# Kernel tuning notes

Hardware: AMD Instinct MI355X
Metric: run time of the kernel (lower is better)

Reference implementation:

```python
import jax, jax.numpy as jnp
import numpy as np

INPUT_SIZE = 512
HIDDEN_SIZE = 1024
OUTPUT_SIZE = 512
BATCH = 128
SEQ_LEN = 512


def setup_inputs() -> dict:
    key = jax.random.key(0)
    k_x, k_xh, k_hh, k_yh = jax.random.split(key, 4)

    def xavier(k, shape):
        fan_in, fan_out = shape
        lim = float(np.sqrt(6.0 / (fan_in + fan_out)))
        return jax.random.uniform(k, shape, jnp.float32, -lim, lim)

    return {
        "x": jax.random.normal(k_x, (BATCH, SEQ_LEN, INPUT_SIZE), jnp.float32),
        "W_xh": xavier(k_xh, (INPUT_SIZE, HIDDEN_SIZE)),
        "W_hh": xavier(k_hh, (HIDDEN_SIZE, HIDDEN_SIZE)),
        "W_yh": xavier(k_yh, (HIDDEN_SIZE, OUTPUT_SIZE)),
        "W_bh": jnp.zeros((HIDDEN_SIZE,), jnp.float32),
        "W_by": jnp.zeros((OUTPUT_SIZE,), jnp.float32),
    }


def reference(x, W_xh, W_hh, W_yh, W_bh, W_by):
    # x: [B, S, I]. Precompute input projections for all steps (parallel GEMM),
    # then scan the strictly sequential hidden recurrence.
    xW = jnp.einsum("bsi,ih->bsh", x, W_xh) + W_bh  # [B, S, H]
    h0 = jnp.zeros((x.shape[0], W_hh.shape[0]), x.dtype)

    def step(h, xw_t):
        h_new = jnp.tanh(xw_t + h @ W_hh)
        return h_new, None

    h_last, _ = jax.lax.scan(step, h0, jnp.swapaxes(xW, 0, 1))  # scan over S
    return h_last @ W_yh + W_by  # [B, O]
```

## Files before the change

kernel.cpp:

```cpp
#include <hip/hip_runtime.h>

typedef _Float16 half8 __attribute__((ext_vector_type(8)));
typedef float f32x4 __attribute__((ext_vector_type(4)));
typedef unsigned long long u64;
typedef u64 u64x2 __attribute__((ext_vector_type(2)));

#define MFMA16(a,b,c) __builtin_amdgcn_mfma_f32_16x16x32_f16((a),(b),(c),0,0,0)

constexpr int B_SZ = 128, S_LEN = 512, I_SZ = 512, H_SZ = 1024, O_SZ = 512;

constexpr size_t XW_OFF   = 0;
constexpr size_t X16_OFF  = XW_OFF   + (size_t)S_LEN * B_SZ * H_SZ * 2;
constexpr size_t WXHT_OFF = X16_OFF  + (size_t)B_SZ * S_LEN * I_SZ * 2;
constexpr size_t WHHT_OFF = WXHT_OFF + (size_t)H_SZ * I_SZ * 2;
constexpr size_t WYHT_OFF = WHHT_OFF + (size_t)H_SZ * H_SZ * 2;
constexpr size_t HB_OFF   = WYHT_OFF + (size_t)O_SZ * H_SZ * 2;
constexpr size_t TAG_OFF  = HB_OFF   + (size_t)8 * 8192 * 8;

__device__ __forceinline__ u64 ag_load64(const u64* p) {
  return __hip_atomic_load(p, __ATOMIC_RELAXED, __HIP_MEMORY_SCOPE_AGENT);
}
__device__ __forceinline__ void ag_store64(u64* p, u64 v) {
  __hip_atomic_store(p, v, __ATOMIC_RELAXED, __HIP_MEMORY_SCOPE_AGENT);
}
__device__ __forceinline__ unsigned ag_load32(const unsigned* p) {
  return __hip_atomic_load(p, __ATOMIC_RELAXED, __HIP_MEMORY_SCOPE_AGENT);
}
__device__ __forceinline__ void ag_store32(unsigned* p, unsigned v) {
  __hip_atomic_store(p, v, __ATOMIC_RELAXED, __HIP_MEMORY_SCOPE_AGENT);
}

__device__ __forceinline__ float ftanh(float z) {
  float e = __builtin_amdgcn_exp2f(z * 2.8853900817779268f);
  return fmaf(-2.f, __builtin_amdgcn_rcpf(e + 1.f), 1.f);
}

__global__ void k_cvt_x(const float* __restrict__ in, _Float16* __restrict__ out) {
  size_t i = ((size_t)blockIdx.x * 256 + threadIdx.x) * 8;
  float4 a = *(const float4*)(in + i);
  float4 b = *(const float4*)(in + i + 4);
  half8 h;
  h[0] = (_Float16)a.x; h[1] = (_Float16)a.y; h[2] = (_Float16)a.z; h[3] = (_Float16)a.w;
  h[4] = (_Float16)b.x; h[5] = (_Float16)b.y; h[6] = (_Float16)b.z; h[7] = (_Float16)b.w;
  *(half8*)(out + i) = h;
}

__global__ void k_transpose_cvt(const float* __restrict__ in, _Float16* __restrict__ out,
                                int K, int N) {
  int k = blockIdx.x * 256 + threadIdx.x;
  int n = blockIdx.y;
  out[(size_t)n * K + k] = (_Float16)in[(size_t)k * N + n];
}

__launch_bounds__(256, 1)
__global__ void k_xw_gemm(const _Float16* __restrict__ A,
                          const _Float16* __restrict__ BT,
                          const float* __restrict__ bias,
                          _Float16* __restrict__ xw)
{
  const int m0 = blockIdx.y * 128;
  const int n0 = blockIdx.x * 128;
  __shared__ __align__(16) _Float16 la[128][72];
  __shared__ __align__(16) _Float16 lb[128][72];
  const int tid = threadIdx.x;
  const int w = tid >> 6, l = tid & 63;
  const int wr = w >> 1, wc = w & 1;
  const int cl = l & 15;
  const int kh = (l >> 4) << 3;
  const int rl = (l >> 4) << 2;

  f32x4 acc[4][4] = {};

  for (int kb = 0; kb < 512; kb += 64) {
    {
      const int r = tid >> 1, sg = tid & 1;
      const _Float16* ga = A  + (size_t)(m0 + r) * 512 + kb + sg * 32;
      const _Float16* gb = BT + (size_t)(n0 + r) * 512 + kb + sg * 32;
      _Float16* da = &la[r][sg * 32];
      _Float16* db = &lb[r][sg * 32];
      #pragma unroll
      for (int i = 0; i < 4; i++) *(half8*)(da + i * 8) = *(const half8*)(ga + i * 8);
      #pragma unroll
      for (int i = 0; i < 4; i++) *(half8*)(db + i * 8) = *(const half8*)(gb + i * 8);
    }
    __syncthreads();
    #pragma unroll
    for (int kk = 0; kk < 64; kk += 32) {
      half8 af[4], bf[4];
      #pragma unroll
      for (int mi = 0; mi < 4; mi++) af[mi] = *(const half8*)(&la[wr * 64 + mi * 16 + cl][kk + kh]);
      #pragma unroll
      for (int ni = 0; ni < 4; ni++) bf[ni] = *(const half8*)(&lb[wc * 64 + ni * 16 + cl][kk + kh]);
      #pragma unroll
      for (int mi = 0; mi < 4; mi++)
        #pragma unroll
        for (int ni = 0; ni < 4; ni++)
          acc[mi][ni] = MFMA16(af[mi], bf[ni], acc[mi][ni]);
    }
    __syncthreads();
  }

  #pragma unroll
  for (int mi = 0; mi < 4; mi++)
    #pragma unroll
    for (int ni = 0; ni < 4; ni++) {
      const int col = n0 + wc * 64 + ni * 16 + cl;
      const float bv = bias[col];
      #pragma unroll
      for (int r = 0; r < 4; r++) {
        const int m = m0 + wr * 64 + mi * 16 + rl + r;
        const int b = m >> 9;
        const int s = m & 511;
        xw[((size_t)(s * B_SZ + b) << 10) + col] = (_Float16)(acc[mi][ni][r] + bv);
      }
    }
}


__device__ __forceinline__ void poll_tags(const unsigned* gtag, int l, unsigned t) {
  for (int it = 0; it < (1 << 17); ++it) {
    unsigned tg = ag_load32(gtag + (l & 31));
    if (__all((int)(tg >= t))) break;
    __builtin_amdgcn_s_sleep(1);
  }
  __builtin_amdgcn_sched_barrier(0);
}

template<int BLK0>
__device__ __forceinline__ void issueq8(u64 (&buf)[8][2], const u64* hrow) {
  #pragma unroll
  for (int b = 0; b < 8; b++) {
    buf[b][0] = ag_load64(hrow + ((BLK0 + b) << 7));
    buf[b][1] = ag_load64(hrow + ((BLK0 + b) << 7) + 1);
  }
}

template<int BLK0>
__device__ __forceinline__ void mfmaq8(const u64 (&buf)[8][2],
                                       const _Float16 (*lw)[1032],
                                       int w, int cl, int kh, f32x4 (&acc)[2][2]) {
  #pragma unroll
  for (int b = 0; b < 8; b++) {
    const int p = BLK0 + b;
    u64x2 w2 = { buf[b][0], buf[b][1] };
    half8 a = __builtin_bit_cast(half8, w2);
    half8 b0 = *(const half8*)&lw[(w << 5) + cl][(p << 5) + kh];
    half8 b1 = *(const half8*)&lw[(w << 5) + 16 + cl][(p << 5) + kh];
    acc[0][p & 1] = MFMA16(a, b0, acc[0][p & 1]);
    acc[1][p & 1] = MFMA16(a, b1, acc[1][p & 1]);
  }
}

template<int BLK0>
__device__ __forceinline__ void mfmaq_o8(const u64 (&buf)[8][2],
                                         const _Float16* bsrc,
                                         int kh, f32x4 (&oa)[2]) {
  #pragma unroll
  for (int b = 0; b < 8; b++) {
    const int p = BLK0 + b;
    u64x2 w2 = { buf[b][0], buf[b][1] };
    half8 a = __builtin_bit_cast(half8, w2);
    half8 bv = *(const half8*)(bsrc + (p << 5) + kh);
    oa[p & 1] = MFMA16(a, bv, oa[p & 1]);
  }
}

__launch_bounds__(128, 1)
__global__ void k_rnn(const _Float16* __restrict__ xw,
                      const _Float16* __restrict__ WhhT,
                      const _Float16* __restrict__ WyhT,
                      const float* __restrict__ Wby,
                      u64* __restrict__ hb,
                      unsigned* __restrict__ tags,
                      float* __restrict__ out)
{
  __shared__ __align__(16) _Float16 lw[64][1032];
  __shared__ __align__(16) _Float16 stb[2][16][40];

  const int bid = blockIdx.x;
  const int g = bid & 7, j = bid >> 3;
  const int tid = threadIdx.x;
  const int w = tid >> 6, l = tid & 63;
  const int p_self = (j << 1) | w;
  const int cl  = l & 15;
  const int kh  = (l >> 4) << 3;
  const int kh2 = (l >> 4) << 1;
  const int rl  = (l >> 4) << 2;
  const int r0  = g << 4;
  const int colbase = p_self << 5;
  unsigned* gtag = tags + (g << 5);
  u64* hbg = hb + ((size_t)g << 13);

  for (int i = tid; i < 64 * 128; i += 128) {
    const int row = i >> 7, c8 = (i & 127) << 3;
    *(half8*)&lw[row][c8] = *(const half8*)&WhhT[((size_t)((j << 6) + row) << 10) + c8];
  }
  __syncthreads();

  for (int t = 0; t < 512; t++) {
    float xv[2][4];
    {
      const _Float16* p = xw + ((size_t)(t * 128 + r0 + rl) << 10) + colbase + cl;
      #pragma unroll
      for (int f = 0; f < 2; f++)
        #pragma unroll
        for (int r = 0; r < 4; r++)
          xv[f][r] = (float)p[((size_t)r << 10) + (f << 4)];
    }

    f32x4 acc[2][2] = {{{}, {}}, {{}, {}}};
    if (t > 0) {
      poll_tags(gtag, l, (unsigned)t);
      const u64* hrow = hbg + ((size_t)(t & 1) << 12) + (cl << 3) + kh2;
      u64 qa[8][2], qb[8][2];
      issueq8<0>(qa, hrow);
      issueq8<8>(qb, hrow);
      mfmaq8<0>(qa, lw, w, cl, kh, acc);
      issueq8<16>(qa, hrow);
      mfmaq8<8>(qb, lw, w, cl, kh, acc);
      issueq8<24>(qb, hrow);
      mfmaq8<16>(qa, lw, w, cl, kh, acc);
      mfmaq8<24>(qb, lw, w, cl, kh, acc);
    }

    #pragma unroll
    for (int f = 0; f < 2; f++)
      #pragma unroll
      for (int r = 0; r < 4; r++) {
        float z = xv[f][r] + acc[f][0][r] + acc[f][1][r];
        stb[w][rl + r][(f << 4) + cl] = (_Float16)ftanh(z);
      }
    asm volatile("s_waitcnt lgkmcnt(0)" ::: "memory");
    __builtin_amdgcn_sched_barrier(0);
    {
      const u64* sp = (const u64*)&stb[w][l >> 2][(l & 3) << 3];
      u64 p0 = sp[0], p1 = sp[1];
      u64* dst = hbg + ((size_t)((t + 1) & 1) << 12) + (p_self << 7)
               + ((l >> 2) << 3) + ((l & 3) << 1);
      ag_store64(dst, p0);
      ag_store64(dst + 1, p1);
    }
    asm volatile("s_waitcnt vmcnt(0)" ::: "memory");
    if (l == 0) ag_store32(gtag + p_self, (unsigned)(t + 1));
  }

  poll_tags(gtag, l, 512u);
  {
    const u64* hrow = hbg + (cl << 3) + kh2;
    const int oc = (p_self << 4) + cl;
    const _Float16* bsrc = WyhT + ((size_t)oc << 10);
    f32x4 oa[2] = {{}, {}};
    u64 qa[8][2], qb[8][2];
    issueq8<0>(qa, hrow);
    issueq8<8>(qb, hrow);
    mfmaq_o8<0>(qa, bsrc, kh, oa);
    issueq8<16>(qa, hrow);
    mfmaq_o8<8>(qb, bsrc, kh, oa);
    issueq8<24>(qb, hrow);
    mfmaq_o8<16>(qa, bsrc, kh, oa);
    mfmaq_o8<24>(qb, bsrc, kh, oa);

    const float bb = Wby[oc];
    #pragma unroll
    for (int r = 0; r < 4; r++)
      out[((size_t)(r0 + rl + r) << 9) + oc] = oa[0][r] + oa[1][r] + bb;
  }
}

extern "C" void kernel_launch(void* const* d_in, const int* in_sizes, int n_in,
                              void* d_out, int out_size, void* d_ws, size_t ws_size,
                              hipStream_t stream) {
  const float* x   = (const float*)d_in[0];
  const float* Wxh = (const float*)d_in[1];
  const float* Whh = (const float*)d_in[2];
  const float* Wyh = (const float*)d_in[3];
  const float* Wbh = (const float*)d_in[4];
  const float* Wby = (const float*)d_in[5];
  float* out = (float*)d_out;

  char* ws = (char*)d_ws;
  _Float16* xw   = (_Float16*)(ws + XW_OFF);
  _Float16* x16  = (_Float16*)(ws + X16_OFF);
  _Float16* WxhT = (_Float16*)(ws + WXHT_OFF);
  _Float16* WhhT = (_Float16*)(ws + WHHT_OFF);
  _Float16* WyhT = (_Float16*)(ws + WYHT_OFF);
  u64*      hb   = (u64*)(ws + HB_OFF);
  unsigned* tags = (unsigned*)(ws + TAG_OFF);

  hipMemsetAsync(tags, 0, 8 * 32 * sizeof(unsigned), stream);

  k_cvt_x<<<16384, 256, 0, stream>>>(x, x16);
  k_transpose_cvt<<<dim3(2, 1024), 256, 0, stream>>>(Wxh, WxhT, 512, 1024);
  k_transpose_cvt<<<dim3(4, 1024), 256, 0, stream>>>(Whh, WhhT, 1024, 1024);
  k_transpose_cvt<<<dim3(4, 512),  256, 0, stream>>>(Wyh, WyhT, 1024, 512);

  k_xw_gemm<<<dim3(8, 512), 256, 0, stream>>>(x16, WxhT, Wbh, xw);

  k_rnn<<<128, 128, 0, stream>>>(xw, WhhT, WyhT, Wby, hb, tags, out);
}
```

Measured before the change: 1.977 ms.

## Consume hidden-state chunks as soon as their producer tags are ready

Replaces the all-or-nothing wait on 32 producer tags with a polling loop that checks readiness per group of 8 producers and issues the loads and MFMAs for each quarter of K as soon as its producers have published step t. Tags are also spread to 64-byte strides so each producer's flag sits on its own cache line, avoiding false sharing between writers. The aim is to overlap recurrent matmul work with waiting on slow blocks in the per-step cross-block barrier. The cost is dynamic control flow, with runtime-indexed helper functions and a polling loop that has no sleep. This may add register pressure and hurt instruction scheduling.

```diff
diff --git a/kernel.cpp b/kernel.cpp
--- a/kernel.cpp
+++ b/kernel.cpp
@@ -117,51 +117,39 @@
 }
 
 
-__device__ __forceinline__ void poll_tags(const unsigned* gtag, int l, unsigned t) {
-  for (int it = 0; it < (1 << 17); ++it) {
-    unsigned tg = ag_load32(gtag + (l & 31));
-    if (__all((int)(tg >= t))) break;
-    __builtin_amdgcn_s_sleep(1);
-  }
-  __builtin_amdgcn_sched_barrier(0);
-}
-
-template<int BLK0>
-__device__ __forceinline__ void issueq8(u64 (&buf)[8][2], const u64* hrow) {
+__device__ __forceinline__ void issueq8r(u64 (&buf)[8][2], const u64* hrow, int blk0) {
   #pragma unroll
   for (int b = 0; b < 8; b++) {
-    buf[b][0] = ag_load64(hrow + ((BLK0 + b) << 7));
-    buf[b][1] = ag_load64(hrow + ((BLK0 + b) << 7) + 1);
-  }
-}
-
-template<int BLK0>
-__device__ __forceinline__ void mfmaq8(const u64 (&buf)[8][2],
-                                       const _Float16 (*lw)[1032],
-                                       int w, int cl, int kh, f32x4 (&acc)[2][2]) {
+    buf[b][0] = ag_load64(hrow + ((blk0 + b) << 7));
+    buf[b][1] = ag_load64(hrow + ((blk0 + b) << 7) + 1);
+  }
+}
+
+__device__ __forceinline__ void mfmaq8r(const u64 (&buf)[8][2],
+                                        const _Float16 (*lw)[1032], int blk0,
+                                        int w, int cl, int kh, f32x4 (&acc)[2][2]) {
   #pragma unroll
   for (int b = 0; b < 8; b++) {
-    const int p = BLK0 + b;
+    const int p = blk0 + b;
     u64x2 w2 = { buf[b][0], buf[b][1] };
     half8 a = __builtin_bit_cast(half8, w2);
     half8 b0 = *(const half8*)&lw[(w << 5) + cl][(p << 5) + kh];
     half8 b1 = *(const half8*)&lw[(w << 5) + 16 + cl][(p << 5) + kh];
-    acc[0][p & 1] = MFMA16(a, b0, acc[0][p & 1]);
-    acc[1][p & 1] = MFMA16(a, b1, acc[1][p & 1]);
-  }
-}
-
-template<int BLK0>
-__device__ __forceinline__ void mfmaq_o8(const u64 (&buf)[8][2],
-                                         const _Float16* bsrc,
-                                         int kh, f32x4 (&oa)[2]) {
+    acc[0][b & 1] = MFMA16(a, b0, acc[0][b & 1]);
+    acc[1][b & 1] = MFMA16(a, b1, acc[1][b & 1]);
+  }
+}
+
+__device__ __forceinline__ void mfmaq_o8r(const u64 (&buf)[8][2],
+                                          const _Float16* bsrc, int blk0,
+                                          int kh, f32x4 (&oa)[2]) {
   #pragma unroll
   for (int b = 0; b < 8; b++) {
-    const int p = BLK0 + b;
+    const int p = blk0 + b;
     u64x2 w2 = { buf[b][0], buf[b][1] };
     half8 a = __builtin_bit_cast(half8, w2);
     half8 bv = *(const half8*)(bsrc + (p << 5) + kh);
-    oa[p & 1] = MFMA16(a, bv, oa[p & 1]);
+    oa[b & 1] = MFMA16(a, bv, oa[b & 1]);
   }
 }
 
@@ -188,7 +176,8 @@
   const int rl  = (l >> 4) << 2;
   const int r0  = g << 4;
   const int colbase = p_self << 5;
-  unsigned* gtag = tags + (g << 5);
+  unsigned* gtag = tags + (g << 9);
+  const unsigned* tp = gtag + ((l & 31) << 4);
   u64* hbg = hb + ((size_t)g << 13);
 
   for (int i = tid; i < 64 * 128; i += 128) {
@@ -210,17 +199,23 @@
 
     f32x4 acc[2][2] = {{{}, {}}, {{}, {}}};
     if (t > 0) {
-      poll_tags(gtag, l, (unsigned)t);
       const u64* hrow = hbg + ((size_t)(t & 1) << 12) + (cl << 3) + kh2;
       u64 qa[8][2], qb[8][2];
-      issueq8<0>(qa, hrow);
-      issueq8<8>(qb, hrow);
-      mfmaq8<0>(qa, lw, w, cl, kh, acc);
-      issueq8<16>(qa, hrow);
-      mfmaq8<8>(qb, lw, w, cl, kh, acc);
-      issueq8<24>(qb, hrow);
-      mfmaq8<16>(qa, lw, w, cl, kh, acc);
-      mfmaq8<24>(qb, lw, w, cl, kh, acc);
+      unsigned done = 0;
+      for (int it = 0; done != 0xFu && it < (1 << 17); ++it) {
+        unsigned tg = ag_load32(tp);
+        unsigned rdy = (unsigned)__ballot((int)(tg >= (unsigned)t));
+        unsigned n01 = 0, n23 = 0;
+        if (!(done & 1u) && ((rdy & 0x000000FFu) == 0x000000FFu)) { issueq8r(qa, hrow, 0);  n01 |= 1u; }
+        if (!(done & 2u) && ((rdy & 0x0000FF00u) == 0x0000FF00u)) { issueq8r(qb, hrow, 8);  n01 |= 2u; }
+        if (n01 & 1u) mfmaq8r(qa, lw, 0,  w, cl, kh, acc);
+        if (n01 & 2u) mfmaq8r(qb, lw, 8,  w, cl, kh, acc);
+        if (!(done & 4u) && ((rdy & 0x00FF0000u) == 0x00FF0000u)) { issueq8r(qa, hrow, 16); n23 |= 1u; }
+        if (!(done & 8u) && ((rdy & 0xFF000000u) == 0xFF000000u)) { issueq8r(qb, hrow, 24); n23 |= 2u; }
+        if (n23 & 1u) mfmaq8r(qa, lw, 16, w, cl, kh, acc);
+        if (n23 & 2u) mfmaq8r(qb, lw, 24, w, cl, kh, acc);
+        done |= (n01 & 3u) | ((n23 & 3u) << 2);
+      }
     }
 
     #pragma unroll
@@ -241,24 +236,29 @@
       ag_store64(dst + 1, p1);
     }
     asm volatile("s_waitcnt vmcnt(0)" ::: "memory");
-    if (l == 0) ag_store32(gtag + p_self, (unsigned)(t + 1));
-  }
-
-  poll_tags(gtag, l, 512u);
+    if (l == 0) ag_store32(gtag + (p_self << 4), (unsigned)(t + 1));
+  }
+
+  for (int it = 0; it < (1 << 17); ++it) {
+    unsigned tg = ag_load32(tp);
+    if (((unsigned)__ballot((int)(tg >= 512u))) == 0xFFFFFFFFu) break;
+    __builtin_amdgcn_s_sleep(1);
+  }
+  __builtin_amdgcn_sched_barrier(0);
   {
     const u64* hrow = hbg + (cl << 3) + kh2;
     const int oc = (p_self << 4) + cl;
     const _Float16* bsrc = WyhT + ((size_t)oc << 10);
     f32x4 oa[2] = {{}, {}};
     u64 qa[8][2], qb[8][2];
-    issueq8<0>(qa, hrow);
-    issueq8<8>(qb, hrow);
-    mfmaq_o8<0>(qa, bsrc, kh, oa);
-    issueq8<16>(qa, hrow);
-    mfmaq_o8<8>(qb, bsrc, kh, oa);
-    issueq8<24>(qb, hrow);
-    mfmaq_o8<16>(qa, bsrc, kh, oa);
-    mfmaq_o8<24>(qb, bsrc, kh, oa);
+    issueq8r(qa, hrow, 0);
+    issueq8r(qb, hrow, 8);
+    mfmaq_o8r(qa, bsrc, 0, kh, oa);
+    issueq8r(qa, hrow, 16);
+    mfmaq_o8r(qb, bsrc, 8, kh, oa);
+    issueq8r(qb, hrow, 24);
+    mfmaq_o8r(qa, bsrc, 16, kh, oa);
+    mfmaq_o8r(qb, bsrc, 24, kh, oa);
 
     const float bb = Wby[oc];
     #pragma unroll
@@ -287,7 +287,7 @@
   u64*      hb   = (u64*)(ws + HB_OFF);
   unsigned* tags = (unsigned*)(ws + TAG_OFF);
 
-  hipMemsetAsync(tags, 0, 8 * 32 * sizeof(unsigned), stream);
+  hipMemsetAsync(tags, 0, 8 * 32 * 16 * sizeof(unsigned), stream);
 
   k_cvt_x<<<16384, 256, 0, stream>>>(x, x16);
   k_transpose_cvt<<<dim3(2, 1024), 256, 0, stream>>>(Wxh, WxhT, 512, 1024);
```

After: 2.109 ms. 6.6% more time.

## Detect same-XCD groups and use L2-coherent sc0 loads for recurrence sync

Applied to the files above, without the earlier changes.

Each block records its XCC ID. If all 16 blocks of a batch group share one XCD, the group switches to a fast path. That path polls tags and loads the hidden state with sc0 global loads, which are coherent within the shared L2. It also batches 16-byte loads before issuing the MFMAs. This aims to cut per-step cross-block synchronization latency compared with agent-scope atomics, and falls back to the old path on a timeout or a mixed-XCD placement. It relies on block-to-XCD placement and on cache-coherence details, so a wrong assumption would make reads stale.

```diff
diff --git a/kernel.cpp b/kernel.cpp
--- a/kernel.cpp
+++ b/kernel.cpp
@@ -16,6 +16,7 @@
 constexpr size_t WYHT_OFF = WHHT_OFF + (size_t)H_SZ * H_SZ * 2;
 constexpr size_t HB_OFF   = WYHT_OFF + (size_t)O_SZ * H_SZ * 2;
 constexpr size_t TAG_OFF  = HB_OFF   + (size_t)8 * 8192 * 8;
+constexpr size_t XCDS_OFF = TAG_OFF  + 1024;
 
 __device__ __forceinline__ u64 ag_load64(const u64* p) {
   return __hip_atomic_load(p, __ATOMIC_RELAXED, __HIP_MEMORY_SCOPE_AGENT);
@@ -28,6 +29,18 @@
 }
 __device__ __forceinline__ void ag_store32(unsigned* p, unsigned v) {
   __hip_atomic_store(p, v, __ATOMIC_RELAXED, __HIP_MEMORY_SCOPE_AGENT);
+}
+
+__device__ __forceinline__ unsigned ld_tag_sc0(const unsigned* p) {
+  unsigned v;
+  asm volatile("global_load_dword %0, %1, off sc0\n\ts_waitcnt vmcnt(0)"
+               : "=v"(v) : "v"(p) : "memory");
+  return v;
+}
+__device__ __forceinline__ u64x2 ld_x4_sc0(const u64* p) {
+  u64x2 v;
+  asm volatile("global_load_dwordx4 %0, %1, off sc0" : "=v"(v) : "v"(p) : "memory");
+  return v;
 }
 
 __device__ __forceinline__ float ftanh(float z) {
@@ -117,7 +130,7 @@
 }
 
 
-__device__ __forceinline__ void poll_tags(const unsigned* gtag, int l, unsigned t) {
+__device__ __forceinline__ void poll_tags_ag(const unsigned* gtag, int l, unsigned t) {
   for (int it = 0; it < (1 << 17); ++it) {
     unsigned tg = ag_load32(gtag + (l & 31));
     if (__all((int)(tg >= t))) break;
@@ -165,6 +178,27 @@
   }
 }
 
+template<int BLK0>
+__device__ __forceinline__ void fast_half(const u64* hrow,
+                                          const _Float16 (*lw)[1032],
+                                          int w, int cl, int kh, f32x4 (&acc)[2][2]) {
+  u64x2 hq[16];
+  #pragma unroll
+  for (int p = 0; p < 16; p++) hq[p] = ld_x4_sc0(hrow + ((BLK0 + p) << 7));
+  asm volatile("s_waitcnt vmcnt(0)" ::: "memory");
+  __builtin_amdgcn_sched_barrier(0);
+  #pragma unroll
+  for (int p = 0; p < 16; p++) {
+    const int pb = BLK0 + p;
+    half8 a  = __builtin_bit_cast(half8, hq[p]);
+    half8 b0 = *(const half8*)&lw[(w << 5) + cl][(pb << 5) + kh];
+    half8 b1 = *(const half8*)&lw[(w << 5) + 16 + cl][(pb << 5) + kh];
+    acc[0][p & 1] = MFMA16(a, b0, acc[0][p & 1]);
+    acc[1][p & 1] = MFMA16(a, b1, acc[1][p & 1]);
+  }
+  __builtin_amdgcn_sched_barrier(0);
+}
+
 __launch_bounds__(128, 1)
 __global__ void k_rnn(const _Float16* __restrict__ xw,
                       const _Float16* __restrict__ WhhT,
@@ -172,6 +206,7 @@
                       const float* __restrict__ Wby,
                       u64* __restrict__ hb,
                       unsigned* __restrict__ tags,
+                      unsigned* __restrict__ xcds,
                       float* __restrict__ out)
 {
   __shared__ __align__(16) _Float16 lw[64][1032];
@@ -189,13 +224,33 @@
   const int r0  = g << 4;
   const int colbase = p_self << 5;
   unsigned* gtag = tags + (g << 5);
+  const unsigned* tp = gtag + (l & 31);
   u64* hbg = hb + ((size_t)g << 13);
+
+  if (tid == 0) {
+    unsigned xcc;
+    asm volatile("s_getreg_b32 %0, hwreg(HW_REG_XCC_ID)" : "=s"(xcc));
+    ag_store32(xcds + (g << 4) + j, (xcc & 7u) + 1u);
+  }
 
   for (int i = tid; i < 64 * 128; i += 128) {
     const int row = i >> 7, c8 = (i & 127) << 3;
     *(half8*)&lw[row][c8] = *(const half8*)&WhhT[((size_t)((j << 6) + row) << 10) + c8];
   }
   __syncthreads();
+
+  bool fast;
+  {
+    unsigned v = 0;
+    bool all_set = false;
+    for (int it = 0; it < (1 << 18) && !all_set; ++it) {
+      v = (l < 16) ? ag_load32(xcds + (g << 4) + l) : 1u;
+      all_set = __all((int)(v != 0u));
+      if (!all_set) __builtin_amdgcn_s_sleep(4);
+    }
+    unsigned v0 = __shfl(v, 0);
+    fast = all_set && __all((int)(l < 16 ? (v == v0) : 1));
+  }
 
   for (int t = 0; t < 512; t++) {
     float xv[2][4];
@@ -210,17 +265,35 @@
 
     f32x4 acc[2][2] = {{{}, {}}, {{}, {}}};
     if (t > 0) {
-      poll_tags(gtag, l, (unsigned)t);
       const u64* hrow = hbg + ((size_t)(t & 1) << 12) + (cl << 3) + kh2;
-      u64 qa[8][2], qb[8][2];
-      issueq8<0>(qa, hrow);
-      issueq8<8>(qb, hrow);
-      mfmaq8<0>(qa, lw, w, cl, kh, acc);
-      issueq8<16>(qa, hrow);
-      mfmaq8<8>(qb, lw, w, cl, kh, acc);
-      issueq8<24>(qb, hrow);
-      mfmaq8<16>(qa, lw, w, cl, kh, acc);
-      mfmaq8<24>(qb, lw, w, cl, kh, acc);
+      bool consumed = false;
+      if (fast) {
+        bool ok = false;
+        for (int it = 0; it < (1 << 14); ++it) {
+          unsigned tg = ld_tag_sc0(tp);
+          if (__all((int)(tg >= (unsigned)t))) { ok = true; break; }
+        }
+        if (ok) {
+          __builtin_amdgcn_sched_barrier(0);
+          fast_half<0>(hrow, lw, w, cl, kh, acc);
+          fast_half<16>(hrow, lw, w, cl, kh, acc);
+          consumed = true;
+        } else {
+          fast = false;
+        }
+      }
+      if (!consumed) {
+        poll_tags_ag(gtag, l, (unsigned)t);
+        u64 qa[8][2], qb[8][2];
+        issueq8<0>(qa, hrow);
+        issueq8<8>(qb, hrow);
+        mfmaq8<0>(qa, lw, w, cl, kh, acc);
+        issueq8<16>(qa, hrow);
+        mfmaq8<8>(qb, lw, w, cl, kh, acc);
+        issueq8<24>(qb, hrow);
+        mfmaq8<16>(qa, lw, w, cl, kh, acc);
+        mfmaq8<24>(qb, lw, w, cl, kh, acc);
+      }
     }
 
     #pragma unroll
@@ -244,7 +317,7 @@
     if (l == 0) ag_store32(gtag + p_self, (unsigned)(t + 1));
   }
 
-  poll_tags(gtag, l, 512u);
+  poll_tags_ag(gtag, l, 512u);
   {
     const u64* hrow = hbg + (cl << 3) + kh2;
     const int oc = (p_self << 4) + cl;
@@ -287,7 +360,7 @@
   u64*      hb   = (u64*)(ws + HB_OFF);
   unsigned* tags = (unsigned*)(ws + TAG_OFF);
 
-  hipMemsetAsync(tags, 0, 8 * 32 * sizeof(unsigned), stream);
+  hipMemsetAsync(tags, 0, 1536, stream);
 
   k_cvt_x<<<16384, 256, 0, stream>>>(x, x16);
   k_transpose_cvt<<<dim3(2, 1024), 256, 0, stream>>>(Wxh, WxhT, 512, 1024);
@@ -296,5 +369,6 @@
 
   k_xw_gemm<<<dim3(8, 512), 256, 0, stream>>>(x16, WxhT, Wbh, xw);
 
-  k_rnn<<<128, 128, 0, stream>>>(xw, WhhT, WyhT, Wby, hb, tags, out);
-}
+  k_rnn<<<128, 128, 0, stream>>>(xw, WhhT, WyhT, Wby, hb, tags,
+                                 (unsigned*)(ws + XCDS_OFF), out);
+}
```

New measurement: 3.050 ms. 1.54x slower.
